# Performance work log

Measured on AMD Instinct MI355X. Metric: run time of the kernel, lower is better.

## Reference

```python
import jax, jax.numpy as jnp
import numpy as np

N_HEADS = 8
WINDOW = 7

def _conv1x1(x, W, b):
    # x: [B,H,W,C]; 1x1 conv == per-pixel matmul
    return jnp.einsum('bhwc,cd->bhwd', x, W) + b

def _to_heads(t, nh):
    # [B,H,W,C] -> channels-first reshape [B, nh, C//nh, H*W] (matches tf transpose+reshape)
    B, H, W, C = t.shape
    return jnp.transpose(t, (0, 3, 1, 2)).reshape(B, nh, C // nh, H * W)

def setup_inputs() -> dict:
    key = jax.random.key(0)
    ks = jax.random.split(key, 8)
    B, H, W, C = 2, 56, 56, 256
    x = jax.random.normal(ks[0], (B, H, W, C), dtype=jnp.float32)
    s = 1.0 / np.sqrt(C)
    Wq = jax.random.normal(ks[1], (C, C), dtype=jnp.float32) * s
    bq = jnp.zeros((C,), dtype=jnp.float32)
    Wk = jax.random.normal(ks[2], (C, C), dtype=jnp.float32) * s
    bk = jnp.zeros((C,), dtype=jnp.float32)
    Wv = jax.random.normal(ks[3], (C, C), dtype=jnp.float32) * s
    bv = jnp.zeros((C,), dtype=jnp.float32)
    # original initializes gamma to 0 (output == x); use small nonzero so the
    # attention path is observable in outputs/grads
    gamma = jax.random.normal(ks[4], (1,), dtype=jnp.float32) * 0.1
    return {"x": x, "Wq": Wq, "bq": bq, "Wk": Wk, "bk": bk, "Wv": Wv, "bv": bv, "gamma": gamma}

def reference(x, Wq, bq, Wk, bk, Wv, bv, gamma):
    B, H, W, C = x.shape
    p = WINDOW // 2
    xp = jnp.pad(x, ((0, 0), (p, p), (p, p), (0, 0)), mode='reflect')  # [B,Hp,Wp,C]
    q = _to_heads(_conv1x1(x, Wq, bq), N_HEADS)    # [B,nh,dk,HW]
    k = _to_heads(_conv1x1(xp, Wk, bk), N_HEADS)   # [B,nh,dk,HpWp]
    v = _to_heads(_conv1x1(xp, Wv, bv), N_HEADS)   # [B,nh,dk,HpWp]
    energy = jnp.einsum('bhdq,bhdk->bhqk', q, k)   # [B,nh,HW,HpWp]
    attn = jax.nn.softmax(energy, axis=-1)
    out = jnp.einsum('bhdk,bhqk->bhdq', v, attn)   # [B,nh,dk,HW]
    out = out.reshape(B, C, H, W).transpose(0, 2, 3, 1)
    return gamma * out + x
```

## Files before the change

### kernel.cpp

```cpp
#include <hip/hip_runtime.h>

typedef unsigned short u16;
typedef float f32x4 __attribute__((ext_vector_type(4)));
typedef short bf16x8 __attribute__((ext_vector_type(8)));
typedef u16 u16x4 __attribute__((ext_vector_type(4)));

__device__ __forceinline__ u16 f2bf(float f) {
    unsigned u = __float_as_uint(f);
    u = (u + 0x7FFFu + ((u >> 16) & 1u)) >> 16;
    return (u16)u;
}

#define LOG2E 1.4426950408889634f

#if __has_builtin(__builtin_amdgcn_exp2f)
__device__ __forceinline__ float exp2_fast(float x) { return __builtin_amdgcn_exp2f(x); }
#else
__device__ __forceinline__ float exp2_fast(float x) { return __expf(x * 0.6931471805599453f); }
#endif

__device__ __forceinline__ unsigned pack2bf(float a, float b) {
    unsigned ua = __float_as_uint(a) + 0x8000u;
    unsigned ub = __float_as_uint(b) + 0x8000u;
#if __has_builtin(__builtin_amdgcn_perm)
    return __builtin_amdgcn_perm(ub, ua, 0x07060302u);
#else
    return ((ua >> 16) & 0xFFFFu) | (ub & 0xFFFF0000u);
#endif
}

#if __has_builtin(__builtin_amdgcn_cvt_pk_bf16_f32)
typedef __bf16 bf2_t __attribute__((ext_vector_type(2)));
__device__ __forceinline__ unsigned cvtpk(float a, float b) {
    bf2_t r = __builtin_amdgcn_cvt_pk_bf16_f32(a, b);
    return __builtin_bit_cast(unsigned, r);
}
#else
__device__ __forceinline__ unsigned cvtpk(float a, float b) { return pack2bf(a, b); }
#endif

__device__ __forceinline__ bf16x8 bc8(uint4 u) { return __builtin_bit_cast(bf16x8, u); }

#if __has_builtin(__builtin_amdgcn_global_load_lds)
typedef const __attribute__((address_space(1))) void* as1cv;
typedef __attribute__((address_space(3))) void* as3v;
__device__ __forceinline__ void dma16(const void* g, void* lds_base, int lane) {
    __builtin_amdgcn_global_load_lds((as1cv)g, (as3v)lds_base, 16, 0, 0);
}
#else
__device__ __forceinline__ void dma16(const void* g, void* lds_base, int lane) {
    *(uint4*)((char*)lds_base + lane * 16) = *(const uint4*)g;
}
#endif

#define BB 2
#define HH 56
#define SQ 3136
#define HP 62
#define SK 3844
#define VT_STRIDE 3856

#define WS_Q    0
#define WS_K    1605632
#define WS_VT   3573760
#define WS_WT   5548032

__global__ __launch_bounds__(256) void wprep_kernel(const float* __restrict__ Wq,
                                                    const float* __restrict__ Wk,
                                                    const float* __restrict__ Wv,
                                                    u16* __restrict__ wtf,
                                                    u16* __restrict__ vtb) {
    int mode = blockIdx.y;
    const float* W = (mode == 0) ? Wq : ((mode == 1) ? Wk : Wv);
    float sc = (mode == 0) ? LOG2E : 1.0f;
    int tid = threadIdx.x;
    int f = blockIdx.x * 8 + (tid >> 5);
    int sub = tid & 31;
    int nz = f >> 6, s = (f >> 3) & 7, nt = f & 7;
#pragma unroll
    for (int e = 0; e < 2; ++e) {
        int L = sub + e * 32;
        int quad = L >> 4, l16 = L & 15;
        int d = nz * 128 + nt * 16 + l16;
        int k0 = s * 32 + quad * 8;
        u16 tmp[8];
#pragma unroll
        for (int j = 0; j < 8; ++j)
            tmp[j] = f2bf(W[(size_t)(k0 + j) * 256 + d] * sc);
        *(uint4*)&wtf[(size_t)mode * 65536 + (size_t)f * 512 + (size_t)L * 8] = *(uint4*)tmp;
    }
    if (mode == 0 && blockIdx.x == 0) {
        for (int i = tid; i < 512 * 12; i += 256) {
            int row = i / 12, col = 3844 + (i - row * 12);
            vtb[(size_t)row * VT_STRIDE + col] = 0;
        }
    }
}

__global__ __launch_bounds__(256, 4) void proj_kernel(const float* __restrict__ x,
                                                      const u16* __restrict__ wtf,
                                                      const float* __restrict__ bq,
                                                      const float* __restrict__ bk,
                                                      const float* __restrict__ bv,
                                                      u16* __restrict__ qout,
                                                      u16* __restrict__ kout,
                                                      u16* __restrict__ vtout) {
    int mode = blockIdx.y, nz = blockIdx.z;
    int mbase = blockIdx.x * 64;
    int M = (mode == 0) ? (BB * SQ) : (BB * SK);
    if (mbase >= M) return;
    int tid = threadIdx.x;
    int wave = tid >> 6, quad = (tid >> 4) & 3, l16 = tid & 15;
    const float* bias = (mode == 0) ? bq : ((mode == 1) ? bk : bv);
    const u16* wf = wtf + (size_t)mode * 65536 + (size_t)nz * 32768 + (size_t)(quad * 16 + l16) * 8;

    int m_a = mbase + wave * 16 + l16;
    if (m_a >= M) m_a = M - 1;
    int xrow;
    if (mode == 0) {
        xrow = m_a;
    } else {
        int bb = (m_a >= SK) ? 1 : 0;
        int sp = m_a - bb * SK;
        int hp = sp / HP, wp = sp - hp * HP;
        int hs = hp - 3; hs = hs < 0 ? -hs : (hs >= HH ? 110 - hs : hs);
        int ws_ = wp - 3; ws_ = ws_ < 0 ? -ws_ : (ws_ >= HH ? 110 - ws_ : ws_);
        xrow = bb * SQ + hs * HH + ws_;
    }
    const float* xr = x + (size_t)xrow * 256;

    f32x4 acc[8];
#pragma unroll
    for (int i = 0; i < 8; i++) acc[i] = (f32x4){0.f, 0.f, 0.f, 0.f};

#pragma unroll
    for (int s = 0; s < 8; ++s) {
        float4 f0 = *(const float4*)&xr[s * 32 + quad * 8];
        float4 f1 = *(const float4*)&xr[s * 32 + quad * 8 + 4];
        uint4 aw = (uint4){pack2bf(f0.x, f0.y), pack2bf(f0.z, f0.w),
                           pack2bf(f1.x, f1.y), pack2bf(f1.z, f1.w)};
        bf16x8 af = bc8(aw);
#pragma unroll
        for (int nt = 0; nt < 8; nt++) {
            bf16x8 bfrag = *(const bf16x8*)&wf[(s * 8 + nt) * 512];
            acc[nt] = __builtin_amdgcn_mfma_f32_16x16x32_bf16(af, bfrag, acc[nt], 0, 0, 0);
        }
    }

    int mrow_base = mbase + wave * 16 + quad * 4;
    if (mode == 2) {
#pragma unroll
        for (int nt = 0; nt < 8; nt++) {
            int c = nz * 128 + nt * 16 + l16;
            float bvv = bias[c];
#pragma unroll
            for (int p = 0; p < 4; p += 2) {
                int m = mrow_base + p;
                if (m + 1 < M) {
                    int bb = (m >= SK) ? 1 : 0;
                    int kp = m - bb * SK;
                    unsigned pk = pack2bf(acc[nt][p] + bvv, acc[nt][p + 1] + bvv);
                    *(unsigned*)&vtout[(size_t)(bb * 256 + c) * VT_STRIDE + kp] = pk;
                }
            }
        }
    } else {
#pragma unroll
        for (int r = 0; r < 4; r++) {
            int m = mrow_base + r;
            if (m >= M) continue;
#pragma unroll
            for (int nt = 0; nt < 8; nt++) {
                int c = nz * 128 + nt * 16 + l16;
                float v = acc[nt][r] + bias[c] * ((mode == 0) ? LOG2E : 1.0f);
                u16 hv = f2bf(v);
                if (mode == 0) qout[((size_t)m << 8) + c] = hv;
                else           kout[((size_t)m << 8) + c] = hv;
            }
        }
    }
}

__global__ __launch_bounds__(256, 3) void attn_kernel(const u16* __restrict__ qb,
                                                      const u16* __restrict__ kb,
                                                      const u16* __restrict__ vtb,
                                                      const float* __restrict__ x,
                                                      const float* __restrict__ gammap,
                                                      float* __restrict__ out) {
    __shared__ __align__(16) u16 S[24576];

    int tid = threadIdx.x;
    int th = tid >> 6, lane = tid & 63, quad = lane >> 4, l16 = lane & 15;
    int bh = blockIdx.x;
    int b = bh >> 3, h = bh & 7;
    int qsub = blockIdx.y * 64;

    bf16x8 qf[4];
#pragma unroll
    for (int i = 0; i < 4; ++i)
        qf[i] = *(const bf16x8*)&qb[((size_t)(b * SQ + qsub + i * 16 + l16) << 8) + h * 32 + quad * 8];

    const u16* kg = kb + ((size_t)(b * SK) << 8) + h * 32;
    const u16* vg = vtb + (size_t)(b * 256 + h * 32) * VT_STRIDE;

    f32x4 o[4][2];
    f32x4 lacc = (f32x4){0.f, 0.f, 0.f, 0.f};
#pragma unroll
    for (int i = 0; i < 4; ++i) {
        o[i][0] = (f32x4){0.f, 0.f, 0.f, 0.f};
        o[i][1] = (f32x4){0.f, 0.f, 0.f, 0.f};
    }

    auto stage = [&](int r_ch, int buf) {
        u16* base = &S[buf * 8192];
        int kbase = r_ch * 128;
#pragma unroll
        for (int i = 0; i < 2; ++i) {
            int g = th + i * 4;
            int grow = kbase + g * 16 + (lane & 15);
            if (grow > SK - 1) grow = SK - 1;
            dma16(kg + ((size_t)grow << 8) + (lane >> 4) * 8, base + g * 512, lane);
            int col = kbase + (2 * g + (lane >> 5)) * 8;
            if (col > VT_STRIDE - 8) col = VT_STRIDE - 8;
            dma16(vg + (size_t)(lane & 31) * VT_STRIDE + col, base + 4096 + g * 512, lane);
        }
    };

    int tA = th, tB = th + 4;
    int vOffA = tA * 512 + (((quad >> 1) * 32 + l16) << 3) + (quad & 1) * 4;
    int vOffB = tB * 512 + (((quad >> 1) * 32 + l16) << 3) + (quad & 1) * 4;

    auto round_body = [&](int bR, bool tail) {
        const u16* Kl = &S[bR * 8192];
        const u16* Vl = Kl + 4096;
        bf16x8 kfA = *(const bf16x8*)&Kl[tA * 512 + lane * 8];
        bf16x8 kfB = *(const bf16x8*)&Kl[tB * 512 + lane * 8];
        uint2 wA0 = *(const uint2*)&Vl[vOffA];
        uint2 wB0 = *(const uint2*)&Vl[vOffB];
        uint2 wA1 = *(const uint2*)&Vl[vOffA + 128];
        uint2 wB1 = *(const uint2*)&Vl[vOffB + 128];
        bf16x8 V0 = bc8((uint4){wA0.x, wA0.y, wB0.x, wB0.y});
        bf16x8 V1 = bc8((uint4){wA1.x, wA1.y, wB1.x, wB1.y});

        f32x4 eA[4], eB[4];
#pragma unroll
        for (int i = 0; i < 4; ++i)
            eA[i] = __builtin_amdgcn_mfma_f32_16x16x32_bf16(kfA, qf[i], (f32x4){0.f, 0.f, 0.f, 0.f}, 0, 0, 0);
#pragma unroll
        for (int i = 0; i < 4; ++i)
            eB[i] = __builtin_amdgcn_mfma_f32_16x16x32_bf16(kfB, qf[i], (f32x4){0.f, 0.f, 0.f, 0.f}, 0, 0, 0);

#pragma unroll
        for (int i = 0; i < 4; ++i) {
            float pA0 = exp2_fast(eA[i][0]), pA1 = exp2_fast(eA[i][1]);
            float pA2 = exp2_fast(eA[i][2]), pA3 = exp2_fast(eA[i][3]);
            float pB0 = exp2_fast(eB[i][0]), pB1 = exp2_fast(eB[i][1]);
            float pB2 = exp2_fast(eB[i][2]), pB3 = exp2_fast(eB[i][3]);
            if (tail) {
                int kA0 = 3840 + tA * 16 + quad * 4;
                pA0 = (kA0 + 0 < SK) ? pA0 : 0.f;
                pA1 = (kA0 + 1 < SK) ? pA1 : 0.f;
                pA2 = (kA0 + 2 < SK) ? pA2 : 0.f;
                pA3 = (kA0 + 3 < SK) ? pA3 : 0.f;
                pB0 = 0.f; pB1 = 0.f; pB2 = 0.f; pB3 = 0.f;
            }
            lacc[i] += ((pA0 + pA1) + (pA2 + pA3)) + ((pB0 + pB1) + (pB2 + pB3));
            bf16x8 pa = bc8((uint4){cvtpk(pA0, pA1), cvtpk(pA2, pA3),
                                    cvtpk(pB0, pB1), cvtpk(pB2, pB3)});
            o[i][0] = __builtin_amdgcn_mfma_f32_16x16x32_bf16(pa, V0, o[i][0], 0, 0, 0);
            o[i][1] = __builtin_amdgcn_mfma_f32_16x16x32_bf16(pa, V1, o[i][1], 0, 0, 0);
        }
    };

    stage(0, 0);
    stage(1, 1);
    int bR = 0, bS = 2;
    for (int r = 0; r < 30; ++r) {
        asm volatile("s_waitcnt vmcnt(4)" ::: "memory");
        if (r + 2 < 31) stage(r + 2, bS);
        round_body(bR, false);
        bR = (bR == 2) ? 0 : bR + 1;
        bS = (bS == 2) ? 0 : bS + 1;
    }
    asm volatile("s_waitcnt vmcnt(0)" ::: "memory");
    round_body(0, true);

    __syncthreads();

    float* mg = (float*)&S[0];
    {
        int slot = ((th & 1) * 64 + lane) * 40;
        if (th >= 2) {
#pragma unroll
            for (int i = 0; i < 4; ++i) {
                *(f32x4*)&mg[slot + i * 8]     = o[i][0];
                *(f32x4*)&mg[slot + i * 8 + 4] = o[i][1];
            }
            *(f32x4*)&mg[slot + 32] = lacc;
        }
        __syncthreads();
        if (th < 2) {
#pragma unroll
            for (int i = 0; i < 4; ++i) {
                o[i][0] += *(const f32x4*)&mg[slot + i * 8];
                o[i][1] += *(const f32x4*)&mg[slot + i * 8 + 4];
            }
            lacc += *(const f32x4*)&mg[slot + 32];
        }
        __syncthreads();
    }
    {
        int slot = lane * 40;
        if (th == 1) {
#pragma unroll
            for (int i = 0; i < 4; ++i) {
                *(f32x4*)&mg[slot + i * 8]     = o[i][0];
                *(f32x4*)&mg[slot + i * 8 + 4] = o[i][1];
            }
            *(f32x4*)&mg[slot + 32] = lacc;
        }
        __syncthreads();
        if (th == 0) {
#pragma unroll
            for (int i = 0; i < 4; ++i) {
                o[i][0] += *(const f32x4*)&mg[slot + i * 8];
                o[i][1] += *(const f32x4*)&mg[slot + i * 8 + 4];
            }
            lacc += *(const f32x4*)&mg[slot + 32];
#pragma unroll
            for (int c = 0; c < 4; ++c) {
                float v = lacc[c];
                v += __shfl_xor(v, 16);
                v += __shfl_xor(v, 32);
                lacc[c] = v;
            }
            float g = gammap[0];
#pragma unroll
            for (int i = 0; i < 4; ++i) {
#pragma unroll
                for (int r2 = 0; r2 < 4; ++r2) {
                    float l = __shfl(lacc[i], quad * 4 + r2);
                    float scl = g / l;
                    int q = qsub + i * 16 + quad * 4 + r2;
                    size_t base = ((size_t)(b * SQ + q) << 8) + h * 32 + l16;
                    out[base]      = o[i][0][r2] * scl + x[base];
                    out[base + 16] = o[i][1][r2] * scl + x[base + 16];
                }
            }
        }
    }
}

extern "C" void kernel_launch(void* const* d_in, const int* in_sizes, int n_in,
                              void* d_out, int out_size, void* d_ws, size_t ws_size,
                              hipStream_t stream) {
    const float* x     = (const float*)d_in[0];
    const float* Wq    = (const float*)d_in[1];
    const float* bq    = (const float*)d_in[2];
    const float* Wk    = (const float*)d_in[3];
    const float* bk    = (const float*)d_in[4];
    const float* Wv    = (const float*)d_in[5];
    const float* bv    = (const float*)d_in[6];
    const float* gamma = (const float*)d_in[7];
    float* out = (float*)d_out;

    u16* ws   = (u16*)d_ws;
    u16* qbuf = ws + WS_Q;
    u16* kbuf = ws + WS_K;
    u16* vtb  = ws + WS_VT;
    u16* wtf  = ws + WS_WT;

    wprep_kernel<<<dim3(16, 3), 256, 0, stream>>>(Wq, Wk, Wv, wtf, vtb);
    proj_kernel<<<dim3(121, 3, 2), 256, 0, stream>>>(x, wtf, bq, bk, bv, qbuf, kbuf, vtb);
    attn_kernel<<<dim3(16, 49), 256, 0, stream>>>(qbuf, kbuf, vtb, x, gamma, out);
}
```

Before: 154.5 us.

## Replace reflect-padded keys with log-multiplicity bias over unique pixels

Reflect padding only duplicates interior pixels, so keys and values are now projected over the 3136 real pixels instead of the 3844 padded ones. Each key's duplicate count enters the softmax as an additive log2 bias through the MFMA accumulator, and padding columns get a large negative bias, which removes about a fifth of the attention rounds and the padded-gather projection work. Row sums now come from an extra MFMA against a ones vector instead of scalar adds and shuffles. The weight-prep kernel transposes through LDS, and the Q/K projection stores packed vectors using swapped MFMA operands.

```diff
diff --git a/kernel.cpp b/kernel.cpp
--- a/kernel.cpp
+++ b/kernel.cpp
@@ -56,43 +56,69 @@
 #define BB 2
 #define HH 56
 #define SQ 3136
-#define HP 62
-#define SK 3844
-#define VT_STRIDE 3856
+#define SKP 3200
+#define VT_STRIDE 3200
 
 #define WS_Q    0
 #define WS_K    1605632
-#define WS_VT   3573760
-#define WS_WT   5548032
+#define WS_VT   3211264
+#define WS_WT   4849664
+#define WS_CB   5046272
 
 __global__ __launch_bounds__(256) void wprep_kernel(const float* __restrict__ Wq,
                                                     const float* __restrict__ Wk,
                                                     const float* __restrict__ Wv,
                                                     u16* __restrict__ wtf,
-                                                    u16* __restrict__ vtb) {
-    int mode = blockIdx.y;
+                                                    u16* __restrict__ vtb,
+                                                    float* __restrict__ cb) {
+    __shared__ u16 T[64][68];
+    int mode = blockIdx.z;
     const float* W = (mode == 0) ? Wq : ((mode == 1) ? Wk : Wv);
     float sc = (mode == 0) ? LOG2E : 1.0f;
+    int kx = blockIdx.x * 64, dx = blockIdx.y * 64;
     int tid = threadIdx.x;
-    int f = blockIdx.x * 8 + (tid >> 5);
-    int sub = tid & 31;
-    int nz = f >> 6, s = (f >> 3) & 7, nt = f & 7;
-#pragma unroll
-    for (int e = 0; e < 2; ++e) {
-        int L = sub + e * 32;
-        int quad = L >> 4, l16 = L & 15;
-        int d = nz * 128 + nt * 16 + l16;
-        int k0 = s * 32 + quad * 8;
+    int r16 = tid >> 4, c4 = (tid & 15) * 4;
+#pragma unroll
+    for (int p = 0; p < 4; ++p) {
+        int kr = p * 16 + r16;
+        float4 f = *(const float4*)&W[(size_t)(kx + kr) * 256 + dx + c4];
+        T[kr][c4 + 0] = f2bf(f.x * sc);
+        T[kr][c4 + 1] = f2bf(f.y * sc);
+        T[kr][c4 + 2] = f2bf(f.z * sc);
+        T[kr][c4 + 3] = f2bf(f.w * sc);
+    }
+    __syncthreads();
+    int l16 = tid & 15, nt_loc = (tid >> 4) & 3, quad = (tid >> 6) & 3;
+#pragma unroll
+    for (int s_loc = 0; s_loc < 2; ++s_loc) {
+        int k0 = s_loc * 32 + quad * 8;
+        int d_loc = nt_loc * 16 + l16;
         u16 tmp[8];
 #pragma unroll
-        for (int j = 0; j < 8; ++j)
-            tmp[j] = f2bf(W[(size_t)(k0 + j) * 256 + d] * sc);
+        for (int j = 0; j < 8; ++j) tmp[j] = T[k0 + j][d_loc];
+        int d = dx + d_loc;
+        int nz = d >> 7, ntg = (d >> 4) & 7;
+        int s = (kx >> 5) + s_loc;
+        int f = (nz * 8 + s) * 8 + ntg;
+        int L = quad * 16 + l16;
         *(uint4*)&wtf[(size_t)mode * 65536 + (size_t)f * 512 + (size_t)L * 8] = *(uint4*)tmp;
     }
-    if (mode == 0 && blockIdx.x == 0) {
-        for (int i = tid; i < 512 * 12; i += 256) {
-            int row = i / 12, col = 3844 + (i - row * 12);
-            vtb[(size_t)row * VT_STRIDE + col] = 0;
+    if (mode == 1 && kx == 0 && dx == 0) {
+        for (int i = tid; i < SKP; i += 256) {
+            float v;
+            if (i < SQ) {
+                int rr = i / 56, cc = i - rr * 56;
+                float a = ((rr >= 1 && rr <= 3) || (rr >= 52 && rr <= 54)) ? 1.f : 0.f;
+                float b2 = ((cc >= 1 && cc <= 3) || (cc >= 52 && cc <= 54)) ? 1.f : 0.f;
+                v = a + b2;
+            } else v = -10000.f;
+            cb[i] = v;
+        }
+    }
+    if (mode == 2 && kx == 0 && dx == 0) {
+        for (int i = tid; i < 512 * 8; i += 256) {
+            int row = i >> 3, c16 = i & 7;
+            *(uint4*)&vtb[(size_t)row * VT_STRIDE + SQ + c16 * 8] = (uint4){0, 0, 0, 0};
         }
     }
 }
@@ -107,27 +133,14 @@
                                                       u16* __restrict__ vtout) {
     int mode = blockIdx.y, nz = blockIdx.z;
     int mbase = blockIdx.x * 64;
-    int M = (mode == 0) ? (BB * SQ) : (BB * SK);
-    if (mbase >= M) return;
     int tid = threadIdx.x;
     int wave = tid >> 6, quad = (tid >> 4) & 3, l16 = tid & 15;
     const float* bias = (mode == 0) ? bq : ((mode == 1) ? bk : bv);
+    float wsc = (mode == 0) ? LOG2E : 1.0f;
     const u16* wf = wtf + (size_t)mode * 65536 + (size_t)nz * 32768 + (size_t)(quad * 16 + l16) * 8;
 
     int m_a = mbase + wave * 16 + l16;
-    if (m_a >= M) m_a = M - 1;
-    int xrow;
-    if (mode == 0) {
-        xrow = m_a;
-    } else {
-        int bb = (m_a >= SK) ? 1 : 0;
-        int sp = m_a - bb * SK;
-        int hp = sp / HP, wp = sp - hp * HP;
-        int hs = hp - 3; hs = hs < 0 ? -hs : (hs >= HH ? 110 - hs : hs);
-        int ws_ = wp - 3; ws_ = ws_ < 0 ? -ws_ : (ws_ >= HH ? 110 - ws_ : ws_);
-        xrow = bb * SQ + hs * HH + ws_;
-    }
-    const float* xr = x + (size_t)xrow * 256;
+    const float* xr = x + (size_t)m_a * 256;
 
     f32x4 acc[8];
 #pragma unroll
@@ -140,15 +153,23 @@
         uint4 aw = (uint4){pack2bf(f0.x, f0.y), pack2bf(f0.z, f0.w),
                            pack2bf(f1.x, f1.y), pack2bf(f1.z, f1.w)};
         bf16x8 af = bc8(aw);
-#pragma unroll
-        for (int nt = 0; nt < 8; nt++) {
-            bf16x8 bfrag = *(const bf16x8*)&wf[(s * 8 + nt) * 512];
-            acc[nt] = __builtin_amdgcn_mfma_f32_16x16x32_bf16(af, bfrag, acc[nt], 0, 0, 0);
-        }
-    }
-
-    int mrow_base = mbase + wave * 16 + quad * 4;
+        if (mode == 2) {
+#pragma unroll
+            for (int nt = 0; nt < 8; nt++) {
+                bf16x8 bfrag = *(const bf16x8*)&wf[(s * 8 + nt) * 512];
+                acc[nt] = __builtin_amdgcn_mfma_f32_16x16x32_bf16(af, bfrag, acc[nt], 0, 0, 0);
+            }
+        } else {
+#pragma unroll
+            for (int nt = 0; nt < 8; nt++) {
+                bf16x8 bfrag = *(const bf16x8*)&wf[(s * 8 + nt) * 512];
+                acc[nt] = __builtin_amdgcn_mfma_f32_16x16x32_bf16(bfrag, af, acc[nt], 0, 0, 0);
+            }
+        }
+    }
+
     if (mode == 2) {
+        int mrow_base = mbase + wave * 16 + quad * 4;
 #pragma unroll
         for (int nt = 0; nt < 8; nt++) {
             int c = nz * 128 + nt * 16 + l16;
@@ -156,27 +177,24 @@
 #pragma unroll
             for (int p = 0; p < 4; p += 2) {
                 int m = mrow_base + p;
-                if (m + 1 < M) {
-                    int bb = (m >= SK) ? 1 : 0;
-                    int kp = m - bb * SK;
-                    unsigned pk = pack2bf(acc[nt][p] + bvv, acc[nt][p + 1] + bvv);
-                    *(unsigned*)&vtout[(size_t)(bb * 256 + c) * VT_STRIDE + kp] = pk;
-                }
+                int bb = (m >= SQ) ? 1 : 0;
+                int kp = m - bb * SQ;
+                unsigned pk = pack2bf(acc[nt][p] + bvv, acc[nt][p + 1] + bvv);
+                *(unsigned*)&vtout[(size_t)(bb * 256 + c) * VT_STRIDE + kp] = pk;
             }
         }
     } else {
-#pragma unroll
-        for (int r = 0; r < 4; r++) {
-            int m = mrow_base + r;
-            if (m >= M) continue;
-#pragma unroll
-            for (int nt = 0; nt < 8; nt++) {
-                int c = nz * 128 + nt * 16 + l16;
-                float v = acc[nt][r] + bias[c] * ((mode == 0) ? LOG2E : 1.0f);
-                u16 hv = f2bf(v);
-                if (mode == 0) qout[((size_t)m << 8) + c] = hv;
-                else           kout[((size_t)m << 8) + c] = hv;
-            }
+        u16* outp = (mode == 0) ? qout : kout;
+#pragma unroll
+        for (int nt = 0; nt < 8; nt++) {
+            int c0 = nz * 128 + nt * 16 + quad * 4;
+            float4 b4 = *(const float4*)&bias[c0];
+            float v0 = acc[nt][0] + b4.x * wsc;
+            float v1 = acc[nt][1] + b4.y * wsc;
+            float v2 = acc[nt][2] + b4.z * wsc;
+            float v3 = acc[nt][3] + b4.w * wsc;
+            uint2 pk = (uint2){pack2bf(v0, v1), pack2bf(v2, v3)};
+            *(uint2*)&outp[((size_t)m_a << 8) + c0] = pk;
         }
     }
 }
@@ -184,6 +202,7 @@
 __global__ __launch_bounds__(256, 3) void attn_kernel(const u16* __restrict__ qb,
                                                       const u16* __restrict__ kb,
                                                       const u16* __restrict__ vtb,
+                                                      const float* __restrict__ cb,
                                                       const float* __restrict__ x,
                                                       const float* __restrict__ gammap,
                                                       float* __restrict__ out) {
@@ -200,16 +219,18 @@
     for (int i = 0; i < 4; ++i)
         qf[i] = *(const bf16x8*)&qb[((size_t)(b * SQ + qsub + i * 16 + l16) << 8) + h * 32 + quad * 8];
 
-    const u16* kg = kb + ((size_t)(b * SK) << 8) + h * 32;
+    const u16* kg = kb + ((size_t)(b * SQ) << 8) + h * 32;
     const u16* vg = vtb + (size_t)(b * 256 + h * 32) * VT_STRIDE;
 
-    f32x4 o[4][2];
-    f32x4 lacc = (f32x4){0.f, 0.f, 0.f, 0.f};
+    f32x4 o[4][2], lv[4];
 #pragma unroll
     for (int i = 0; i < 4; ++i) {
         o[i][0] = (f32x4){0.f, 0.f, 0.f, 0.f};
         o[i][1] = (f32x4){0.f, 0.f, 0.f, 0.f};
-    }
+        lv[i]   = (f32x4){0.f, 0.f, 0.f, 0.f};
+    }
+    short ov = (short)0x3F80;
+    bf16x8 ones8 = {ov, ov, ov, ov, ov, ov, ov, ov};
 
     auto stage = [&](int r_ch, int buf) {
         u16* base = &S[buf * 8192];
@@ -218,10 +239,9 @@
         for (int i = 0; i < 2; ++i) {
             int g = th + i * 4;
             int grow = kbase + g * 16 + (lane & 15);
-            if (grow > SK - 1) grow = SK - 1;
+            if (grow > SQ - 1) grow = SQ - 1;
             dma16(kg + ((size_t)grow << 8) + (lane >> 4) * 8, base + g * 512, lane);
             int col = kbase + (2 * g + (lane >> 5)) * 8;
-            if (col > VT_STRIDE - 8) col = VT_STRIDE - 8;
             dma16(vg + (size_t)(lane & 31) * VT_STRIDE + col, base + 4096 + g * 512, lane);
         }
     };
@@ -230,11 +250,13 @@
     int vOffA = tA * 512 + (((quad >> 1) * 32 + l16) << 3) + (quad & 1) * 4;
     int vOffB = tB * 512 + (((quad >> 1) * 32 + l16) << 3) + (quad & 1) * 4;
 
-    auto round_body = [&](int bR, bool tail) {
+    auto round_body = [&](int r, int bR) {
         const u16* Kl = &S[bR * 8192];
         const u16* Vl = Kl + 4096;
         bf16x8 kfA = *(const bf16x8*)&Kl[tA * 512 + lane * 8];
         bf16x8 kfB = *(const bf16x8*)&Kl[tB * 512 + lane * 8];
+        f32x4 cfA = __builtin_bit_cast(f32x4, *(const float4*)&cb[r * 128 + tA * 16 + quad * 4]);
+        f32x4 cfB = __builtin_bit_cast(f32x4, *(const float4*)&cb[r * 128 + tB * 16 + quad * 4]);
         uint2 wA0 = *(const uint2*)&Vl[vOffA];
         uint2 wB0 = *(const uint2*)&Vl[vOffB];
         uint2 wA1 = *(const uint2*)&Vl[vOffA + 128];
@@ -245,10 +267,10 @@
         f32x4 eA[4], eB[4];
 #pragma unroll
         for (int i = 0; i < 4; ++i)
-            eA[i] = __builtin_amdgcn_mfma_f32_16x16x32_bf16(kfA, qf[i], (f32x4){0.f, 0.f, 0.f, 0.f}, 0, 0, 0);
+            eA[i] = __builtin_amdgcn_mfma_f32_16x16x32_bf16(kfA, qf[i], cfA, 0, 0, 0);
 #pragma unroll
         for (int i = 0; i < 4; ++i)
-            eB[i] = __builtin_amdgcn_mfma_f32_16x16x32_bf16(kfB, qf[i], (f32x4){0.f, 0.f, 0.f, 0.f}, 0, 0, 0);
+            eB[i] = __builtin_amdgcn_mfma_f32_16x16x32_bf16(kfB, qf[i], cfB, 0, 0, 0);
 
 #pragma unroll
         for (int i = 0; i < 4; ++i) {
@@ -256,47 +278,39 @@
             float pA2 = exp2_fast(eA[i][2]), pA3 = exp2_fast(eA[i][3]);
             float pB0 = exp2_fast(eB[i][0]), pB1 = exp2_fast(eB[i][1]);
             float pB2 = exp2_fast(eB[i][2]), pB3 = exp2_fast(eB[i][3]);
-            if (tail) {
-                int kA0 = 3840 + tA * 16 + quad * 4;
-                pA0 = (kA0 + 0 < SK) ? pA0 : 0.f;
-                pA1 = (kA0 + 1 < SK) ? pA1 : 0.f;
-                pA2 = (kA0 + 2 < SK) ? pA2 : 0.f;
-                pA3 = (kA0 + 3 < SK) ? pA3 : 0.f;
-                pB0 = 0.f; pB1 = 0.f; pB2 = 0.f; pB3 = 0.f;
-            }
-            lacc[i] += ((pA0 + pA1) + (pA2 + pA3)) + ((pB0 + pB1) + (pB2 + pB3));
             bf16x8 pa = bc8((uint4){cvtpk(pA0, pA1), cvtpk(pA2, pA3),
                                     cvtpk(pB0, pB1), cvtpk(pB2, pB3)});
             o[i][0] = __builtin_amdgcn_mfma_f32_16x16x32_bf16(pa, V0, o[i][0], 0, 0, 0);
             o[i][1] = __builtin_amdgcn_mfma_f32_16x16x32_bf16(pa, V1, o[i][1], 0, 0, 0);
+            lv[i]   = __builtin_amdgcn_mfma_f32_16x16x32_bf16(pa, ones8, lv[i], 0, 0, 0);
         }
     };
 
     stage(0, 0);
     stage(1, 1);
     int bR = 0, bS = 2;
-    for (int r = 0; r < 30; ++r) {
+    for (int r = 0; r < 24; ++r) {
         asm volatile("s_waitcnt vmcnt(4)" ::: "memory");
-        if (r + 2 < 31) stage(r + 2, bS);
-        round_body(bR, false);
+        if (r + 2 < 25) stage(r + 2, bS);
+        round_body(r, bR);
         bR = (bR == 2) ? 0 : bR + 1;
         bS = (bS == 2) ? 0 : bS + 1;
     }
     asm volatile("s_waitcnt vmcnt(0)" ::: "memory");
-    round_body(0, true);
+    round_body(24, bR);
 
     __syncthreads();
 
     float* mg = (float*)&S[0];
     {
-        int slot = ((th & 1) * 64 + lane) * 40;
+        int slot = ((th & 1) * 64 + lane) * 48;
         if (th >= 2) {
 #pragma unroll
             for (int i = 0; i < 4; ++i) {
-                *(f32x4*)&mg[slot + i * 8]     = o[i][0];
-                *(f32x4*)&mg[slot + i * 8 + 4] = o[i][1];
-            }
-            *(f32x4*)&mg[slot + 32] = lacc;
+                *(f32x4*)&mg[slot + i * 8]      = o[i][0];
+                *(f32x4*)&mg[slot + i * 8 + 4]  = o[i][1];
+                *(f32x4*)&mg[slot + 32 + i * 4] = lv[i];
+            }
         }
         __syncthreads();
         if (th < 2) {
@@ -304,43 +318,32 @@
             for (int i = 0; i < 4; ++i) {
                 o[i][0] += *(const f32x4*)&mg[slot + i * 8];
                 o[i][1] += *(const f32x4*)&mg[slot + i * 8 + 4];
-            }
-            lacc += *(const f32x4*)&mg[slot + 32];
+                lv[i]   += *(const f32x4*)&mg[slot + 32 + i * 4];
+            }
         }
         __syncthreads();
     }
     {
-        int slot = lane * 40;
+        int slot = lane * 48;
         if (th == 1) {
 #pragma unroll
             for (int i = 0; i < 4; ++i) {
-                *(f32x4*)&mg[slot + i * 8]     = o[i][0];
-                *(f32x4*)&mg[slot + i * 8 + 4] = o[i][1];
-            }
-            *(f32x4*)&mg[slot + 32] = lacc;
+                *(f32x4*)&mg[slot + i * 8]      = o[i][0];
+                *(f32x4*)&mg[slot + i * 8 + 4]  = o[i][1];
+                *(f32x4*)&mg[slot + 32 + i * 4] = lv[i];
+            }
         }
         __syncthreads();
         if (th == 0) {
+            float g = gammap[0];
 #pragma unroll
             for (int i = 0; i < 4; ++i) {
                 o[i][0] += *(const f32x4*)&mg[slot + i * 8];
                 o[i][1] += *(const f32x4*)&mg[slot + i * 8 + 4];
-            }
-            lacc += *(const f32x4*)&mg[slot + 32];
-#pragma unroll
-            for (int c = 0; c < 4; ++c) {
-                float v = lacc[c];
-                v += __shfl_xor(v, 16);
-                v += __shfl_xor(v, 32);
-                lacc[c] = v;
-            }
-            float g = gammap[0];
-#pragma unroll
-            for (int i = 0; i < 4; ++i) {
+                lv[i]   += *(const f32x4*)&mg[slot + 32 + i * 4];
 #pragma unroll
                 for (int r2 = 0; r2 < 4; ++r2) {
-                    float l = __shfl(lacc[i], quad * 4 + r2);
-                    float scl = g / l;
+                    float scl = g / lv[i][r2];
                     int q = qsub + i * 16 + quad * 4 + r2;
                     size_t base = ((size_t)(b * SQ + q) << 8) + h * 32 + l16;
                     out[base]      = o[i][0][r2] * scl + x[base];
@@ -369,8 +372,9 @@
     u16* kbuf = ws + WS_K;
     u16* vtb  = ws + WS_VT;
     u16* wtf  = ws + WS_WT;
-
-    wprep_kernel<<<dim3(16, 3), 256, 0, stream>>>(Wq, Wk, Wv, wtf, vtb);
-    proj_kernel<<<dim3(121, 3, 2), 256, 0, stream>>>(x, wtf, bq, bk, bv, qbuf, kbuf, vtb);
-    attn_kernel<<<dim3(16, 49), 256, 0, stream>>>(qbuf, kbuf, vtb, x, gamma, out);
-}
+    float* cbias = (float*)(ws + WS_CB);
+
+    wprep_kernel<<<dim3(4, 4, 3), 256, 0, stream>>>(Wq, Wk, Wv, wtf, vtb, cbias);
+    proj_kernel<<<dim3(98, 3, 2), 256, 0, stream>>>(x, wtf, bq, bk, bv, qbuf, kbuf, vtb);
+    attn_kernel<<<dim3(16, 49), 256, 0, stream>>>(qbuf, kbuf, vtb, cbias, x, gamma, out);
+}
```

New measurement: 156.9 us. Within noise of the previous version (+1.5%).
